# Kernel tuning notes

Measured on AMD Instinct MI355X. Metric: run time of the kernel, lower is better.

## Reference

```python
import jax, jax.numpy as jnp
import numpy as np

HEAD_DIM = 64
N_HEADS = 16
D_MODEL = 2048
SEQ = 2048
BATCH = 1
LAYER_IDX = 12
LN_EPS = 1e-5


def setup_inputs() -> dict:
    key = jax.random.key(0)
    ks = jax.random.split(key, 8)
    s = 0.02
    return {
        "x": jax.random.normal(ks[0], (BATCH, SEQ, D_MODEL), dtype=jnp.float32),
        "W_qkv": jax.random.normal(ks[1], (3 * N_HEADS * 2 * HEAD_DIM, D_MODEL), dtype=jnp.float32) * s,
        "W_o": jax.random.normal(ks[2], (D_MODEL, D_MODEL), dtype=jnp.float32) * s,
        "lambda_q1": jax.random.normal(ks[3], (2 * HEAD_DIM,), dtype=jnp.float32) * 0.1,
        "lambda_k1": jax.random.normal(ks[4], (2 * HEAD_DIM,), dtype=jnp.float32) * 0.1,
        "lambda_q2": jax.random.normal(ks[5], (2 * HEAD_DIM,), dtype=jnp.float32) * 0.1,
        "lambda_k2": jax.random.normal(ks[6], (2 * HEAD_DIM,), dtype=jnp.float32) * 0.1,
        "gn_gamma": jnp.ones((N_HEADS, 2 * HEAD_DIM), dtype=jnp.float32),
        "gn_beta": jnp.zeros((N_HEADS, 2 * HEAD_DIM), dtype=jnp.float32),
    }


def _causal_sdpa(q, k, v, scale):
    # q,k: [B,H,S,d], v: [B,H,S,2d]
    S = q.shape[2]
    scores = jnp.einsum("bhqd,bhkd->bhqk", q, k) * scale
    causal = jnp.tril(jnp.ones((S, S), dtype=bool))
    scores = jnp.where(causal[None, None], scores, jnp.float32(-1e30))
    attn = jax.nn.softmax(scores, axis=-1)
    return jnp.einsum("bhqk,bhkd->bhqd", attn, v)


def reference(x, W_qkv, W_o, lambda_q1, lambda_k1, lambda_q2, lambda_k2, gn_gamma, gn_beta):
    B, S, D = x.shape
    lambda_init = 0.8 - 0.6 * jnp.exp(jnp.float32(-0.3 * LAYER_IDX))
    scale = HEAD_DIM ** -0.5

    qkv = x @ W_qkv.T  # [B,S,6*H*d]
    qkv = qkv.reshape(B, S, 3, N_HEADS, 2 * HEAD_DIM)
    q = jnp.transpose(qkv[:, :, 0], (0, 2, 1, 3))  # [B,H,S,2d]
    k = jnp.transpose(qkv[:, :, 1], (0, 2, 1, 3))
    v = jnp.transpose(qkv[:, :, 2], (0, 2, 1, 3))
    q1, q2 = q[..., :HEAD_DIM], q[..., HEAD_DIM:]
    k1, k2 = k[..., :HEAD_DIM], k[..., HEAD_DIM:]

    lam = jnp.exp(lambda_q1 * lambda_k1) - jnp.exp(lambda_q2 * lambda_k2) + lambda_init  # [2d]

    A1 = _causal_sdpa(q1, k1, v, scale)
    A2 = _causal_sdpa(q2, k2, v, scale)
    out = A1 - lam * A2  # broadcast over value channel [B,H,S,2d]

    # per-head LayerNorm over last dim
    mu = jnp.mean(out, axis=-1, keepdims=True)
    var = jnp.mean((out - mu) ** 2, axis=-1, keepdims=True)
    out = (out - mu) * jax.lax.rsqrt(var + LN_EPS)
    out = out * gn_gamma[None, :, None, :] + gn_beta[None, :, None, :]

    out = out * (1.0 - lambda_init)
    out = jnp.transpose(out, (0, 2, 1, 3)).reshape(B, S, D)
    return out @ W_o.T
```

## Files before the change

### kernel.cpp

```cpp
#include <hip/hip_runtime.h>

typedef short short8 __attribute__((ext_vector_type(8)));
typedef float f32x4 __attribute__((ext_vector_type(4)));
typedef unsigned short u16;
typedef u16 u16x8 __attribute__((ext_vector_type(8)));
typedef u16 u16x4 __attribute__((ext_vector_type(4)));

__device__ static inline u16 f2bf(float f) {
    union { float f; unsigned u; } v; v.f = f;
    unsigned r = v.u + 0x7fffu + ((v.u >> 16) & 1u);
    return (u16)(r >> 16);
}

__device__ static inline unsigned cvt_pk_bf16(float a, float b) {
    unsigned r;
    asm("v_cvt_pk_bf16_f32 %0, %1, %2" : "=v"(r) : "v"(a), "v"(b));
    return r;
}

__device__ static inline void gload16(const u16* g, u16* l) {
    __builtin_amdgcn_global_load_lds(
        (const __attribute__((address_space(1))) unsigned int*)g,
        (__attribute__((address_space(3))) unsigned int*)l,
        16, 0, 0);
}

__global__ __launch_bounds__(256) void cast_kernel(const float* __restrict__ in,
                                                   u16* __restrict__ out, int n) {
    int i = (blockIdx.x * 256 + threadIdx.x) * 4;
    if (i + 3 < n) {
        f32x4 v = *(const f32x4*)&in[i];
        u16x4 o;
        o[0] = f2bf(v[0]); o[1] = f2bf(v[1]); o[2] = f2bf(v[2]); o[3] = f2bf(v[3]);
        *(u16x4*)&out[i] = o;
    }
}

template <int BM, int BN, int MODE, int MINW>
__global__ __launch_bounds__(256, MINW) void gemm_bt(const u16* __restrict__ A,
                                                     const u16* __restrict__ B,
                                                     int M, int N, int K,
                                                     float* __restrict__ C,
                                                     u16* __restrict__ Qo,
                                                     u16* __restrict__ Ko,
                                                     u16* __restrict__ Vo) {
    constexpr int APT = BM * 4 / 256;
    constexpr int BPT = BN * 4 / 256;
    constexpr int MT = BM / 32, NT = BN / 32;
    __shared__ u16 As[BM * 32];
    __shared__ u16 Bs[BN * 32];
    const int tid  = threadIdx.x;
    const int lane = tid & 63, wave = tid >> 6;
    const int quad = lane >> 4, l15 = lane & 15;
    const int wm = wave >> 1, wn = wave & 1;
    const int m0 = blockIdx.y * BM;
    const int n0 = blockIdx.x * BN;

    f32x4 acc[MT][NT] = {};

    const u16* aga[APT];
    const u16* bga[BPT];
#pragma unroll
    for (int i = 0; i < APT; i++) {
        int s = tid + i * 256, r = s >> 2;
        int kg = (s & 3) ^ ((r >> 1) & 3);
        aga[i] = &A[(size_t)(m0 + r) * K + kg * 8];
    }
#pragma unroll
    for (int i = 0; i < BPT; i++) {
        int s = tid + i * 256, r = s >> 2;
        int kg = (s & 3) ^ ((r >> 1) & 3);
        bga[i] = &B[(size_t)(n0 + r) * K + kg * 8];
    }

    for (int k0 = 0; k0 < K; k0 += 32) {
        if (k0) __syncthreads();
#pragma unroll
        for (int i = 0; i < APT; i++)
            gload16(aga[i] + k0, &As[(wave * 64 + i * 256) * 8]);
#pragma unroll
        for (int i = 0; i < BPT; i++)
            gload16(bga[i] + k0, &Bs[(wave * 64 + i * 256) * 8]);
        __syncthreads();

        short8 af[MT], bf[NT];
#pragma unroll
        for (int mt = 0; mt < MT; mt++) {
            int row = wm * (BM / 2) + mt * 16 + l15;
            int slot = row * 4 + (quad ^ ((row >> 1) & 3));
            af[mt] = *(const short8*)&As[slot * 8];
        }
#pragma unroll
        for (int nt = 0; nt < NT; nt++) {
            int row = wn * (BN / 2) + nt * 16 + l15;
            int slot = row * 4 + (quad ^ ((row >> 1) & 3));
            bf[nt] = *(const short8*)&Bs[slot * 8];
        }
#pragma unroll
        for (int mt = 0; mt < MT; mt++)
#pragma unroll
            for (int nt = 0; nt < NT; nt++)
                acc[mt][nt] = __builtin_amdgcn_mfma_f32_16x16x32_bf16(af[mt], bf[nt], acc[mt][nt], 0, 0, 0);
    }

    if (MODE == 0) {
#pragma unroll
        for (int mt = 0; mt < MT; mt++)
#pragma unroll
            for (int nt = 0; nt < NT; nt++)
#pragma unroll
                for (int r = 0; r < 4; r++) {
                    int row = m0 + wm * (BM / 2) + mt * 16 + quad * 4 + r;
                    int col = n0 + wn * (BN / 2) + nt * 16 + l15;
                    C[(size_t)row * N + col] = acc[mt][nt][r];
                }
    } else {
        const int comp = n0 >> 11, h = (n0 >> 7) & 15;
        u16* dst = (comp == 0) ? Qo : ((comp == 1) ? Ko : Vo);
        const float sc = (comp == 0) ? 0.18033688f : 1.0f;
#pragma unroll
        for (int mt = 0; mt < MT; mt++)
#pragma unroll
            for (int nt = 0; nt < NT; nt++)
#pragma unroll
                for (int r = 0; r < 4; r++) {
                    int row = m0 + wm * (BM / 2) + mt * 16 + quad * 4 + r;
                    int d = wn * (BN / 2) + nt * 16 + l15;
                    dst[((h * 2048) + row) * 128 + d] = f2bf(acc[mt][nt][r] * sc);
                }
    }
}

__global__ __launch_bounds__(256) void transpose_v(const u16* __restrict__ vb,
                                                   u16* __restrict__ vT) {
    __shared__ u16 T[64 * 136];
    const int s0 = blockIdx.x * 64, h = blockIdx.y;
    const int tid = threadIdx.x;
#pragma unroll
    for (int i = 0; i < 4; i++) {
        int c = tid + i * 256;
        int s = c >> 4, dch = c & 15;
        *(u16x8*)&T[s * 136 + dch * 8] =
            *(const u16x8*)&vb[((h * 2048) + s0 + s) * 128 + dch * 8];
    }
    __syncthreads();
#pragma unroll
    for (int i = 0; i < 4; i++) {
        int c = tid + i * 256;
        int d = c >> 3, sch = c & 7;
        u16x8 o;
#pragma unroll
        for (int j = 0; j < 8; j++) o[j] = T[(sch * 8 + j) * 136 + d];
        *(u16x8*)&vT[((h * 128) + d) * 2048 + s0 + sch * 8] = o;
    }
}

__global__ __launch_bounds__(256, 2) void attn_kernel(const u16* __restrict__ qb,
                                                      const u16* __restrict__ kb,
                                                      const u16* __restrict__ vT,
                                                      float* __restrict__ ob) {
    const int bid = blockIdx.x;
    const int h = bid & 15;
    const int comp = (bid >> 4) & 1;
    const int j = bid >> 5;
    const int J = (j < 8) ? (2 * j + 1) : (30 - 2 * j);
    const int nkt = 2 * J + 2;
    const int q0 = J * 128;
    const int tid = threadIdx.x, lane = tid & 63, wave = tid >> 6;
    const int quad = lane >> 4, l15 = lane & 15;
    const int qh = quad >> 1, ql = quad & 1;

    __shared__ u16 Ks[64 * 64];
    __shared__ u16 VsT[128 * 64];
    const char* KsB = (const char*)Ks;
    const char* VsB = (const char*)VsT;

    const u16* kb_h = &kb[(size_t)h * 2048 * 128 + comp * 64];
    const u16* vT_h = &vT[(size_t)h * 128 * 2048];

    const int c1 = tid, c2 = tid + 256;
    const int k1key = c1 >> 3, k1dc = ((c1 & 7) ^ k1key) & 7;
    const int k2key = c2 >> 3, k2dc = ((c2 & 7) ^ k2key) & 7;
    const u16* kaddr1 = &kb_h[k1key * 128 + k1dc * 8];
    const u16* kaddr2 = &kb_h[k2key * 128 + k2dc * 8];
    const u16* vaddr[4];
#pragma unroll
    for (int i = 0; i < 4; i++) {
        int c = tid + i * 256;
        int dim = c >> 3, kc = ((c & 7) ^ dim) & 7;
        vaddr[i] = &vT_h[dim * 2048 + kc * 8];
    }

    const int koff0 = l15 * 128 + ((quad ^ l15) & 7) * 16;
    const int koff1 = l15 * 128 + (((quad + 4) ^ l15) & 7) * 16;
    int vb[8][2];
#pragma unroll
    for (int nt = 0; nt < 8; nt++) {
        int dim = nt * 16 + l15;
        int base = dim * 128 + ((qh ^ dim) & 7) * 16 + ql * 8;
        vb[nt][0] = base;
        vb[nt][1] = base ^ 64;
    }

    short8 aq[2][2];
#pragma unroll
    for (int qs = 0; qs < 2; qs++)
#pragma unroll
        for (int ks = 0; ks < 2; ks++) {
            int qrow = q0 + wave * 32 + qs * 16 + l15;
            aq[qs][ks] = *(const short8*)
                &qb[((h * 2048) + qrow) * 128 + comp * 64 + ks * 32 + quad * 8];
        }

    float l_acc[2] = {0.f, 0.f};
    f32x4 acc[8][2] = {};

    u16x8 kst0, kst1, vst[4];
    kst0 = *(const u16x8*)kaddr1;
    kst1 = *(const u16x8*)kaddr2;
#pragma unroll
    for (int i = 0; i < 4; i++) vst[i] = *(const u16x8*)vaddr[i];
    const u16* kp1 = kaddr1 + 8192;
    const u16* kp2 = kaddr2 + 8192;
    const u16* vp[4];
#pragma unroll
    for (int i = 0; i < 4; i++) vp[i] = vaddr[i] + 64;

    for (int kt = 0; kt < nkt; kt++) {
        *(u16x8*)&Ks[c1 * 8] = kst0;
        *(u16x8*)&Ks[c2 * 8] = kst1;
#pragma unroll
        for (int i = 0; i < 4; i++) *(u16x8*)&VsT[(tid + i * 256) * 8] = vst[i];
        __syncthreads();

        if (kt + 1 < nkt) {
            kst0 = *(const u16x8*)kp1; kp1 += 8192;
            kst1 = *(const u16x8*)kp2; kp2 += 8192;
#pragma unroll
            for (int i = 0; i < 4; i++) { vst[i] = *(const u16x8*)vp[i]; vp[i] += 64; }
        }

        short8 kf[4][2];
#pragma unroll
        for (int kn = 0; kn < 4; kn++) {
            kf[kn][0] = *(const short8*)(KsB + (koff0 + kn * 2048));
            kf[kn][1] = *(const short8*)(KsB + (koff1 + kn * 2048));
        }

        short8 b8[2][2];
#pragma unroll
        for (int qs = 0; qs < 2; qs++) {
#pragma unroll
            for (int kn2 = 0; kn2 < 2; kn2++) {
                f32x4 sa = {}, sb = {};
                sa = __builtin_amdgcn_mfma_f32_16x16x32_bf16(kf[2 * kn2][0], aq[qs][0], sa, 0, 0, 0);
                sa = __builtin_amdgcn_mfma_f32_16x16x32_bf16(kf[2 * kn2][1], aq[qs][1], sa, 0, 0, 0);
                sb = __builtin_amdgcn_mfma_f32_16x16x32_bf16(kf[2 * kn2 + 1][0], aq[qs][0], sb, 0, 0, 0);
                sb = __builtin_amdgcn_mfma_f32_16x16x32_bf16(kf[2 * kn2 + 1][1], aq[qs][1], sb, 0, 0, 0);
                if (kt >= nkt - 2) {
                    int q = q0 + wave * 32 + qs * 16 + l15;
                    int kb0 = kt * 64 + kn2 * 32 + quad * 4;
#pragma unroll
                    for (int r = 0; r < 4; r++) {
                        if (kb0 + r > q) sa[r] = -1e30f;
                        if (kb0 + 16 + r > q) sb[r] = -1e30f;
                    }
                }
                float p0 = exp2f(sa[0]), p1 = exp2f(sa[1]), p2 = exp2f(sa[2]), p3 = exp2f(sa[3]);
                float p4 = exp2f(sb[0]), p5 = exp2f(sb[1]), p6 = exp2f(sb[2]), p7 = exp2f(sb[3]);
                l_acc[qs] += ((p0 + p1) + (p2 + p3)) + ((p4 + p5) + (p6 + p7));
                union { unsigned w[4]; short8 s; } pw;
                pw.w[0] = cvt_pk_bf16(p0, p1);
                pw.w[1] = cvt_pk_bf16(p2, p3);
                pw.w[2] = cvt_pk_bf16(p4, p5);
                pw.w[3] = cvt_pk_bf16(p6, p7);
                b8[qs][kn2] = pw.s;
            }
        }

        __builtin_amdgcn_s_setprio(1);
#pragma unroll
        for (int nt = 0; nt < 8; nt++) {
#pragma unroll
            for (int kn2 = 0; kn2 < 2; kn2++) {
                union { u16x4 h4[2]; short8 s; } av;
                int o0 = vb[nt][kn2];
                av.h4[0] = *(const u16x4*)(VsB + o0);
                av.h4[1] = *(const u16x4*)(VsB + (o0 ^ 32));
                acc[nt][0] = __builtin_amdgcn_mfma_f32_16x16x32_bf16(av.s, b8[0][kn2], acc[nt][0], 0, 0, 0);
                acc[nt][1] = __builtin_amdgcn_mfma_f32_16x16x32_bf16(av.s, b8[1][kn2], acc[nt][1], 0, 0, 0);
            }
        }
        __builtin_amdgcn_s_setprio(0);
        __syncthreads();
    }

#pragma unroll
    for (int qs = 0; qs < 2; qs++) {
        l_acc[qs] += __shfl_xor(l_acc[qs], 16);
        l_acc[qs] += __shfl_xor(l_acc[qs], 32);
    }
    float rl[2] = {1.f / l_acc[0], 1.f / l_acc[1]};

#pragma unroll
    for (int qs = 0; qs < 2; qs++) {
        int s = q0 + wave * 32 + qs * 16 + l15;
        float* orow = &ob[((size_t)(comp * 16 + h) * 2048 + s) * 128 + quad * 4];
#pragma unroll
        for (int nt = 0; nt < 8; nt++) {
            f32x4 v;
#pragma unroll
            for (int r = 0; r < 4; r++) v[r] = acc[nt][qs][r] * rl[qs];
            *(f32x4*)&orow[nt * 16] = v;
        }
    }
}

__global__ __launch_bounds__(256) void combine_kernel(const float* __restrict__ ob,
                                                      const float* __restrict__ lq1,
                                                      const float* __restrict__ lk1,
                                                      const float* __restrict__ lq2,
                                                      const float* __restrict__ lk2,
                                                      const float* __restrict__ gamma,
                                                      const float* __restrict__ beta,
                                                      u16* __restrict__ attn) {
    const int tid = threadIdx.x, wave = tid >> 6, lane = tid & 63;
    const int row = blockIdx.x * 4 + wave;
    const int s = row >> 4, h = row & 15;
    const float lambda_init = 0.8f - 0.6f * __expf(-3.6f);
    const int d0 = lane * 2;
    float vals[2];
#pragma unroll
    for (int j = 0; j < 2; j++) {
        int d = d0 + j;
        float a1 = ob[((h)*2048 + s) * 128 + d];
        float a2 = ob[((16 + h) * 2048 + s) * 128 + d];
        float lam = __expf(lq1[d] * lk1[d]) - __expf(lq2[d] * lk2[d]) + lambda_init;
        vals[j] = a1 - lam * a2;
    }
    float sum = vals[0] + vals[1];
    float sq = vals[0] * vals[0] + vals[1] * vals[1];
#pragma unroll
    for (int off = 1; off < 64; off <<= 1) {
        sum += __shfl_xor(sum, off);
        sq += __shfl_xor(sq, off);
    }
    float mu = sum * (1.f / 128.f);
    float var = sq * (1.f / 128.f) - mu * mu;
    float rinv = rsqrtf(var + 1e-5f);
    float osc = 1.f - lambda_init;
#pragma unroll
    for (int j = 0; j < 2; j++) {
        int d = d0 + j;
        float g = gamma[h * 128 + d], b = beta[h * 128 + d];
        float v = ((vals[j] - mu) * rinv * g + b) * osc;
        attn[s * 2048 + h * 128 + d] = f2bf(v);
    }
}

extern "C" void kernel_launch(void* const* d_in, const int* in_sizes, int n_in,
                              void* d_out, int out_size, void* d_ws, size_t ws_size,
                              hipStream_t stream) {
    (void)in_sizes; (void)n_in; (void)out_size; (void)ws_size;
    const float* x    = (const float*)d_in[0];
    const float* Wqkv = (const float*)d_in[1];
    const float* Wo   = (const float*)d_in[2];
    const float* lq1  = (const float*)d_in[3];
    const float* lk1  = (const float*)d_in[4];
    const float* lq2  = (const float*)d_in[5];
    const float* lk2  = (const float*)d_in[6];
    const float* gam  = (const float*)d_in[7];
    const float* bet  = (const float*)d_in[8];
    float* out = (float*)d_out;

    char* ws = (char*)d_ws;
    u16*   xb    = (u16*)(ws);
    u16*   wqkvb = (u16*)(ws + (size_t)(8 << 20));
    float* ob    = (float*)(ws + (size_t)(8 << 20));
    u16*   wob   = (u16*)(ws + (size_t)(40 << 20));
    u16*   qb    = (u16*)(ws + (size_t)(48 << 20));
    u16*   kb    = (u16*)(ws + (size_t)(56 << 20));
    u16*   vb    = (u16*)(ws + (size_t)(64 << 20));
    u16*   vT    = (u16*)(ws + (size_t)(72 << 20));
    u16*   attn  = (u16*)(ws);

    cast_kernel<<<(2048 * 2048) / 1024, 256, 0, stream>>>(x, xb, 2048 * 2048);
    cast_kernel<<<(6144 * 2048) / 1024, 256, 0, stream>>>(Wqkv, wqkvb, 6144 * 2048);
    cast_kernel<<<(2048 * 2048) / 1024, 256, 0, stream>>>(Wo, wob, 2048 * 2048);
    gemm_bt<128, 128, 1, 3><<<dim3(48, 16), 256, 0, stream>>>(
        xb, wqkvb, 2048, 6144, 2048, nullptr, qb, kb, vb);
    transpose_v<<<dim3(32, 16), 256, 0, stream>>>(vb, vT);
    attn_kernel<<<512, 256, 0, stream>>>(qb, kb, vT, ob);
    combine_kernel<<<8192, 256, 0, stream>>>(ob, lq1, lk1, lq2, lk2, gam, bet, attn);
    gemm_bt<128, 64, 0, 2><<<dim3(32, 16), 256, 0, stream>>>(
        attn, wob, 2048, 2048, 2048, out, nullptr, nullptr, nullptr);
}
```

Before: 300.1 us.

## Add dedicated 256x256-tile QKV GEMM with double-buffered LDS pipeline

Replaces the generic 128x128 QKV projection GEMM with a specialised 512-thread kernel that computes 256x256 output tiles, using a K-step of 64 split into two 32-wide halves, double-buffered LDS with direct global-to-LDS loads, XOR-swizzled LDS layout and raised wave priority around MFMA blocks. Larger tiles raise arithmetic intensity and cut global reloads, and interleaving loads with MFMAs hides memory latency. In exchange it uses 128KB of LDS per block and many accumulator registers, and the grid shrinks to 192 blocks, which may underfill the GPU's CUs. The epilogue keeps the Q scaling and the head-major scatter into Q/K/V.

New measurement: 301.8 us. No clear change (+0.6%).

```diff
diff --git a/kernel.cpp b/kernel.cpp
--- a/kernel.cpp
+++ b/kernel.cpp
@@ -34,6 +34,149 @@
         o[0] = f2bf(v[0]); o[1] = f2bf(v[1]); o[2] = f2bf(v[2]); o[3] = f2bf(v[3]);
         *(u16x4*)&out[i] = o;
     }
+}
+
+__global__ __launch_bounds__(512, 2) void gemm_qkv256(const u16* __restrict__ A,
+                                                      const u16* __restrict__ B,
+                                                      u16* __restrict__ Qo,
+                                                      u16* __restrict__ Ko,
+                                                      u16* __restrict__ Vo) {
+    constexpr int K = 2048;
+    constexpr int NTILE = K / 64;
+    __shared__ u16 Asm[2][2][256 * 32];
+    __shared__ u16 Bsm[2][2][256 * 32];
+    const int tid = threadIdx.x;
+    const int lane = tid & 63, wave = tid >> 6;
+    const int quad = lane >> 4, l15 = lane & 15;
+    const int wm = wave >> 2, wn = wave & 3;
+    const int bid = blockIdx.x;
+    const int by = bid & 7, bx = bid >> 3;
+    const int m0 = by * 256, n0 = bx * 256;
+
+    const u16* aga[2];
+    const u16* bga[2];
+#pragma unroll
+    for (int j = 0; j < 2; j++) {
+        int s = tid + j * 512, r = s >> 2;
+        int kg = (s & 3) ^ ((r >> 1) & 3);
+        aga[j] = &A[(size_t)(m0 + r) * K + kg * 8];
+        bga[j] = &B[(size_t)(n0 + r) * K + kg * 8];
+    }
+    const int ld0 = (wave * 64) * 8;
+    const int ld1 = (512 + wave * 64) * 8;
+
+    f32x4 acc[8][4] = {};
+
+    gload16(aga[0], &Asm[0][0][ld0]);
+    gload16(aga[1], &Asm[0][0][ld1]);
+    gload16(bga[0], &Bsm[0][0][ld0]);
+    gload16(bga[1], &Bsm[0][0][ld1]);
+    gload16(aga[0] + 32, &Asm[0][1][ld0]);
+    gload16(aga[1] + 32, &Asm[0][1][ld1]);
+    gload16(bga[0] + 32, &Bsm[0][1][ld0]);
+    gload16(bga[1] + 32, &Bsm[0][1][ld1]);
+
+    for (int t = 0; t < NTILE; t++) {
+        const int p = t & 1, pn = p ^ 1;
+        const int tn = (t + 1 < NTILE) ? t + 1 : t;
+        const int ko = tn * 64;
+
+        asm volatile("s_waitcnt vmcnt(4)\n\ts_barrier" ::: "memory");
+        gload16(aga[0] + ko, &Asm[pn][0][ld0]);
+        gload16(aga[1] + ko, &Asm[pn][0][ld1]);
+
+        short8 b0[4], a[4];
+#pragma unroll
+        for (int nf = 0; nf < 4; nf++) {
+            int row = wn * 64 + nf * 16 + l15;
+            int slot = quad ^ ((row >> 1) & 3);
+            b0[nf] = *(const short8*)&Bsm[p][0][row * 32 + slot * 8];
+        }
+#pragma unroll
+        for (int mf = 0; mf < 4; mf++) {
+            int row = wm * 128 + mf * 16 + l15;
+            int slot = quad ^ ((row >> 1) & 3);
+            a[mf] = *(const short8*)&Asm[p][0][row * 32 + slot * 8];
+        }
+        __builtin_amdgcn_s_setprio(1);
+#pragma unroll
+        for (int mf = 0; mf < 4; mf++)
+#pragma unroll
+            for (int nf = 0; nf < 4; nf++)
+                acc[mf][nf] = __builtin_amdgcn_mfma_f32_16x16x32_bf16(a[mf], b0[nf], acc[mf][nf], 0, 0, 0);
+        __builtin_amdgcn_s_setprio(0);
+
+        gload16(bga[0] + ko, &Bsm[pn][0][ld0]);
+        gload16(bga[1] + ko, &Bsm[pn][0][ld1]);
+#pragma unroll
+        for (int mf = 0; mf < 4; mf++) {
+            int row = wm * 128 + (mf + 4) * 16 + l15;
+            int slot = quad ^ ((row >> 1) & 3);
+            a[mf] = *(const short8*)&Asm[p][0][row * 32 + slot * 8];
+        }
+        __builtin_amdgcn_s_setprio(1);
+#pragma unroll
+        for (int mf = 0; mf < 4; mf++)
+#pragma unroll
+            for (int nf = 0; nf < 4; nf++)
+                acc[mf + 4][nf] = __builtin_amdgcn_mfma_f32_16x16x32_bf16(a[mf], b0[nf], acc[mf + 4][nf], 0, 0, 0);
+        __builtin_amdgcn_s_setprio(0);
+
+        asm volatile("s_waitcnt vmcnt(4)\n\ts_barrier" ::: "memory");
+        gload16(aga[0] + ko + 32, &Asm[pn][1][ld0]);
+        gload16(aga[1] + ko + 32, &Asm[pn][1][ld1]);
+
+#pragma unroll
+        for (int nf = 0; nf < 4; nf++) {
+            int row = wn * 64 + nf * 16 + l15;
+            int slot = quad ^ ((row >> 1) & 3);
+            b0[nf] = *(const short8*)&Bsm[p][1][row * 32 + slot * 8];
+        }
+#pragma unroll
+        for (int mf = 0; mf < 4; mf++) {
+            int row = wm * 128 + mf * 16 + l15;
+            int slot = quad ^ ((row >> 1) & 3);
+            a[mf] = *(const short8*)&Asm[p][1][row * 32 + slot * 8];
+        }
+        __builtin_amdgcn_s_setprio(1);
+#pragma unroll
+        for (int mf = 0; mf < 4; mf++)
+#pragma unroll
+            for (int nf = 0; nf < 4; nf++)
+                acc[mf][nf] = __builtin_amdgcn_mfma_f32_16x16x32_bf16(a[mf], b0[nf], acc[mf][nf], 0, 0, 0);
+        __builtin_amdgcn_s_setprio(0);
+
+        gload16(bga[0] + ko + 32, &Bsm[pn][1][ld0]);
+        gload16(bga[1] + ko + 32, &Bsm[pn][1][ld1]);
+#pragma unroll
+        for (int mf = 0; mf < 4; mf++) {
+            int row = wm * 128 + (mf + 4) * 16 + l15;
+            int slot = quad ^ ((row >> 1) & 3);
+            a[mf] = *(const short8*)&Asm[p][1][row * 32 + slot * 8];
+        }
+        __builtin_amdgcn_s_setprio(1);
+#pragma unroll
+        for (int mf = 0; mf < 4; mf++)
+#pragma unroll
+            for (int nf = 0; nf < 4; nf++)
+                acc[mf + 4][nf] = __builtin_amdgcn_mfma_f32_16x16x32_bf16(a[mf], b0[nf], acc[mf + 4][nf], 0, 0, 0);
+        __builtin_amdgcn_s_setprio(0);
+    }
+
+    const int comp = bx >> 3;
+    u16* dst = (comp == 0) ? Qo : ((comp == 1) ? Ko : Vo);
+    const float sc = (comp == 0) ? 0.18033688f : 1.0f;
+#pragma unroll
+    for (int mf = 0; mf < 8; mf++)
+#pragma unroll
+        for (int nf = 0; nf < 4; nf++)
+#pragma unroll
+            for (int r = 0; r < 4; r++) {
+                int row = m0 + wm * 128 + mf * 16 + quad * 4 + r;
+                int d = (n0 & 2047) + wn * 64 + nf * 16 + l15;
+                int h = d >> 7, dd = d & 127;
+                dst[((h * 2048) + row) * 128 + dd] = f2bf(acc[mf][nf][r] * sc);
+            }
 }
 
 template <int BM, int BN, int MODE, int MINW>
@@ -387,8 +530,7 @@
     cast_kernel<<<(2048 * 2048) / 1024, 256, 0, stream>>>(x, xb, 2048 * 2048);
     cast_kernel<<<(6144 * 2048) / 1024, 256, 0, stream>>>(Wqkv, wqkvb, 6144 * 2048);
     cast_kernel<<<(2048 * 2048) / 1024, 256, 0, stream>>>(Wo, wob, 2048 * 2048);
-    gemm_bt<128, 128, 1, 3><<<dim3(48, 16), 256, 0, stream>>>(
-        xb, wqkvb, 2048, 6144, 2048, nullptr, qb, kb, vb);
+    gemm_qkv256<<<192, 512, 0, stream>>>(xb, wqkvb, qb, kb, vb);
     transpose_v<<<dim3(32, 16), 256, 0, stream>>>(vb, vT);
     attn_kernel<<<512, 256, 0, stream>>>(qb, kb, vT, ob);
     combine_kernel<<<8192, 256, 0, stream>>>(ob, lq1, lk1, lq2, lk2, gam, bet, attn);
```
